# Performance work log

Hardware: AMD Instinct MI355X
Metric: run time of the kernel (lower is better)

The kernel has to match this reference:

```python
import jax, jax.numpy as jnp
import numpy as np

B, N, D, U = 8, 2048, 512, 128


def setup_inputs() -> dict:
    key = jax.random.key(0)
    k_x, k_q, k_k, k_v, k_o = jax.random.split(key, 5)
    scale_in = 1.0 / np.sqrt(D)
    scale_u = 1.0 / np.sqrt(U)
    return {
        "inputs": jax.random.normal(k_x, (B, N, D), dtype=jnp.float32),
        "W_q": jax.random.normal(k_q, (D, U), dtype=jnp.float32) * scale_in,
        "W_k": jax.random.normal(k_k, (D, U), dtype=jnp.float32) * scale_in,
        "W_v": jax.random.normal(k_v, (D, U), dtype=jnp.float32) * scale_in,
        "W_o": jax.random.normal(k_o, (U, D), dtype=jnp.float32) * scale_u,
        "b_o": jnp.zeros((D,), dtype=jnp.float32),
    }


def reference(inputs, W_q, W_k, W_v, W_o, b_o):
    # Single-head scaled dot-product self-attention + output dense + residual
    Q = jnp.einsum('bnd,du->bnu', inputs, W_q)
    K = jnp.einsum('bnd,du->bnu', inputs, W_k)
    V = jnp.einsum('bnd,du->bnu', inputs, W_v)
    inv_sqrt_u = 1.0 / jnp.sqrt(jnp.asarray(W_q.shape[-1], inputs.dtype))
    scores = jnp.einsum('bnu,bmu->bnm', Q, K) * inv_sqrt_u  # [B,N,N]
    attn = jax.nn.softmax(scores, axis=-1)
    ctx = jnp.einsum('bnm,bmu->bnu', attn, V)  # [B,N,U]
    return jnp.einsum('bnu,ud->bnd', ctx, W_o) + b_o + inputs
```

## Files before the change

kernel.cpp:

```cpp
#include <hip/hip_runtime.h>

#define BB 8
#define NN 2048
#define DD 512
#define UU 128
#define SPLITS 4
#define KSPLIT 512

typedef __bf16 bf16_t;
typedef __bf16 bf16x4 __attribute__((ext_vector_type(4)));
typedef __bf16 bf16x8 __attribute__((ext_vector_type(8)));
typedef float floatx4 __attribute__((ext_vector_type(4)));

__device__ __forceinline__ floatx4 mfma16(bf16x8 a, bf16x8 b, floatx4 c) {
  return __builtin_amdgcn_mfma_f32_16x16x32_bf16(a, b, c, 0, 0, 0);
}

#define SW(r, g) ((((g) ^ ((r) & 7)) * 8))

__device__ __forceinline__ void gld_lds16(const bf16_t* g, bf16_t* l) {
  __builtin_amdgcn_global_load_lds(
      (const __attribute__((address_space(1))) unsigned int*)g,
      (__attribute__((address_space(3))) unsigned int*)l, 16, 0, 0);
}

__global__ __launch_bounds__(256) void cast_x_kernel(const float* __restrict__ x,
                                                     bf16_t* __restrict__ xb) {
  int G = blockIdx.x * 256 + threadIdx.x;
  int token = G >> 6;
  int g = G & 63;
  int dstg = (g & 56) | ((g & 7) ^ (token & 7));
  const float4* src = reinterpret_cast<const float4*>(x) + (size_t)G * 2;
  float4 a = src[0], b = src[1];
  bf16x8 o;
  o[0] = (bf16_t)a.x; o[1] = (bf16_t)a.y; o[2] = (bf16_t)a.z; o[3] = (bf16_t)a.w;
  o[4] = (bf16_t)b.x; o[5] = (bf16_t)b.y; o[6] = (bf16_t)b.z; o[7] = (bf16_t)b.w;
  *reinterpret_cast<bf16x8*>(&xb[(size_t)token * 512 + dstg * 8]) = o;
}

__global__ __launch_bounds__(256) void pack_w_kernel(const float* __restrict__ wq,
                                                     const float* __restrict__ wk,
                                                     const float* __restrict__ wv,
                                                     const float* __restrict__ wo,
                                                     bf16_t* __restrict__ wqkvt,
                                                     bf16_t* __restrict__ wot) {
  int gid = blockIdx.x * 256 + threadIdx.x;
  if (gid < 384 * 512) {
    int nrow = gid >> 9;
    int kdst = gid & 511;
    int ksrc = (kdst & ~56) | (((((kdst >> 3) & 7)) ^ (nrow & 7)) << 3);
    const float* src = (nrow < 128) ? wq : ((nrow < 256) ? wk : wv);
    int n = nrow & 127;
    wqkvt[gid] = (bf16_t)src[ksrc * 128 + n];
  } else {
    int g = gid - 384 * 512;
    int nrow = g >> 7;
    int kdst = g & 127;
    int ksrc = (kdst & ~56) | (((((kdst >> 3) & 7)) ^ (nrow & 7)) << 3);
    wot[g] = (bf16_t)wo[ksrc * 512 + nrow];
  }
}

__global__ __launch_bounds__(256, 4) void qkv_gemm_kernel(const bf16_t* __restrict__ xb,
                                                          const bf16_t* __restrict__ wqkvt,
                                                          bf16_t* __restrict__ Q,
                                                          bf16_t* __restrict__ K,
                                                          bf16_t* __restrict__ Vt) {
  __shared__ bf16_t lA[128 * 64];
  __shared__ bf16_t lB[64 * 64];
  const int m0 = blockIdx.x * 128;
  const int n0 = blockIdx.y * 64;
  const int tid = threadIdx.x;
  const int w = tid >> 6, lane = tid & 63;
  const int quad = lane >> 4, l15 = lane & 15;

  floatx4 zero4 = {0.f, 0.f, 0.f, 0.f};
  floatx4 acc[2][4];
#pragma unroll
  for (int mi = 0; mi < 2; mi++)
#pragma unroll
    for (int nt = 0; nt < 4; nt++) acc[mi][nt] = zero4;

  for (int kc = 0; kc < 512; kc += 64) {
    __syncthreads();
#pragma unroll
    for (int i = 0; i < 4; i++) {
      int t = tid + i * 256;
      int r = t >> 3, g = t & 7;
      gld_lds16(&xb[(size_t)(m0 + r) * 512 + kc + g * 8], &lA[t * 8]);
    }
#pragma unroll
    for (int i = 0; i < 2; i++) {
      int t = tid + i * 256;
      int r = t >> 3, g = t & 7;
      gld_lds16(&wqkvt[(size_t)(n0 + r) * 512 + kc + g * 8], &lB[t * 8]);
    }
    asm volatile("s_waitcnt vmcnt(0)" ::: "memory");
    __syncthreads();
#pragma unroll
    for (int kb = 0; kb < 2; kb++) {
      bf16x8 bfr[4];
#pragma unroll
      for (int nt = 0; nt < 4; nt++)
        bfr[nt] = *reinterpret_cast<const bf16x8*>(
            &lB[(nt * 16 + l15) * 64 + SW(l15, kb * 4 + quad)]);
#pragma unroll
      for (int mi = 0; mi < 2; mi++) {
        bf16x8 a = *reinterpret_cast<const bf16x8*>(
            &lA[(w * 32 + mi * 16 + l15) * 64 + SW(l15, kb * 4 + quad)]);
#pragma unroll
        for (int nt = 0; nt < 4; nt++)
          acc[mi][nt] = mfma16(a, bfr[nt], acc[mi][nt]);
      }
    }
  }

#pragma unroll
  for (int mi = 0; mi < 2; mi++)
#pragma unroll
    for (int nt = 0; nt < 4; nt++) {
      int n = n0 + nt * 16 + l15;
#pragma unroll
      for (int r = 0; r < 4; r++) {
        int token = m0 + w * 32 + mi * 16 + quad * 4 + r;
        bf16_t h = (bf16_t)acc[mi][nt][r];
        if (n < 128) {
          Q[(size_t)token * 128 + n] = h;
        } else if (n < 256) {
          int nk = n - 128;
          int nsw = (nk & ~56) | ((((nk >> 3) & 7) ^ (token & 7)) << 3);
          K[(size_t)token * 128 + nsw] = h;
        } else {
          int bidx = token >> 11;
          int t = token & 2047;
          int u = n - 256;
          int tsw = (t & ~56) | ((((t >> 3) & 7) ^ (u & 7)) << 3);
          Vt[((size_t)bidx * 128 + u) * 2048 + tsw] = h;
        }
      }
    }
}

__global__ __launch_bounds__(256, 2) void attn_kernel(const bf16_t* __restrict__ Q,
                                                      const bf16_t* __restrict__ K,
                                                      const bf16_t* __restrict__ Vt,
                                                      bf16_t* __restrict__ Op,
                                                      float* __restrict__ ml) {
  __shared__ bf16_t lK[2][64 * 128];
  __shared__ bf16_t lV[2][128 * 64];
  __shared__ bf16_t lP[4][32 * 64];

  const int b = blockIdx.y;
  const int qb = blockIdx.x;
  const int s = blockIdx.z;
  const int tid = threadIdx.x;
  const int w = tid >> 6, lane = tid & 63;
  const int quad = lane >> 4, l15 = lane & 15;
  const float c = 0.08838834764831845f * 1.4426950408889634f;

  bf16x8 qf[2][4];
#pragma unroll
  for (int mt = 0; mt < 2; mt++) {
    const bf16_t* qrow =
        &Q[((size_t)b * NN + qb * 128 + w * 32 + mt * 16 + l15) * 128 + quad * 8];
#pragma unroll
    for (int kb = 0; kb < 4; kb++)
      qf[mt][kb] = *reinterpret_cast<const bf16x8*>(qrow + kb * 32);
  }

  float l_part[2] = {0.f, 0.f};
  floatx4 zero4 = {0.f, 0.f, 0.f, 0.f};
  floatx4 accO[2][8];
#pragma unroll
  for (int mt = 0; mt < 2; mt++)
#pragma unroll
    for (int ut = 0; ut < 8; ut++) accO[mt][ut] = zero4;

  bf16_t* pw = &lP[w][0];
  const int kt0 = s * KSPLIT;
  const bf16_t* kbase = &K[(size_t)b * NN * 128];
  const bf16_t* vbase = &Vt[(size_t)b * 128 * 2048];

  {
    const bf16_t* ksrc = kbase + (size_t)kt0 * 128;
#pragma unroll
    for (int i = 0; i < 4; i++) {
      int t = tid + i * 256;
      gld_lds16(ksrc + (size_t)t * 8, &lK[0][t * 8]);
    }
#pragma unroll
    for (int i = 0; i < 4; i++) {
      int t = tid + i * 256;
      int r = t >> 3, g = t & 7;
      gld_lds16(vbase + (size_t)r * 2048 + kt0 + g * 8, &lV[0][t * 8]);
    }
  }
  asm volatile("s_waitcnt vmcnt(0)" ::: "memory");
  __syncthreads();

  int cur = 0;
  for (int kt = kt0; kt < kt0 + KSPLIT; kt += 64) {
    if (kt + 64 < kt0 + KSPLIT) {
      const int nxt = kt + 64;
      const bf16_t* ksrc = kbase + (size_t)nxt * 128;
#pragma unroll
      for (int i = 0; i < 4; i++) {
        int t = tid + i * 256;
        gld_lds16(ksrc + (size_t)t * 8, &lK[cur ^ 1][t * 8]);
      }
#pragma unroll
      for (int i = 0; i < 4; i++) {
        int t = tid + i * 256;
        int r = t >> 3, g = t & 7;
        gld_lds16(vbase + (size_t)r * 2048 + nxt + g * 8, &lV[cur ^ 1][t * 8]);
      }
    }

    floatx4 accS[4][2];
#pragma unroll
    for (int km = 0; km < 4; km++)
#pragma unroll
      for (int mt = 0; mt < 2; mt++) accS[km][mt] = zero4;
    __builtin_amdgcn_s_setprio(1);
#pragma unroll
    for (int kb = 0; kb < 4; kb++) {
#pragma unroll
      for (int km = 0; km < 4; km++) {
        bf16x8 kf = *reinterpret_cast<const bf16x8*>(
            &lK[cur][(km * 16 + l15) * 128 + SW(l15, kb * 4 + quad)]);
#pragma unroll
        for (int mt = 0; mt < 2; mt++)
          accS[km][mt] = mfma16(kf, qf[mt][kb], accS[km][mt]);
      }
    }
    __builtin_amdgcn_s_setprio(0);

#pragma unroll
    for (int km = 0; km < 4; km++) {
#pragma unroll
      for (int mt = 0; mt < 2; mt++) {
        float p0 = __builtin_amdgcn_exp2f(accS[km][mt][0] * c);
        float p1 = __builtin_amdgcn_exp2f(accS[km][mt][1] * c);
        float p2 = __builtin_amdgcn_exp2f(accS[km][mt][2] * c);
        float p3 = __builtin_amdgcn_exp2f(accS[km][mt][3] * c);
        l_part[mt] += (p0 + p1) + (p2 + p3);
        bf16x4 pk;
        pk[0] = (bf16_t)p0; pk[1] = (bf16_t)p1; pk[2] = (bf16_t)p2; pk[3] = (bf16_t)p3;
        int row = mt * 16 + l15;
        int g = km * 2 + (quad >> 1);
        *reinterpret_cast<bf16x4*>(
            &pw[row * 64 + ((g ^ (row & 7)) * 8) + (quad & 1) * 4]) = pk;
      }
    }
    asm volatile("s_waitcnt lgkmcnt(0)" ::: "memory");

    __builtin_amdgcn_s_setprio(1);
#pragma unroll
    for (int kb = 0; kb < 2; kb++) {
      bf16x8 pa[2];
#pragma unroll
      for (int mt = 0; mt < 2; mt++)
        pa[mt] = *reinterpret_cast<const bf16x8*>(
            &pw[(mt * 16 + l15) * 64 + SW(l15, kb * 4 + quad)]);
#pragma unroll
      for (int ut = 0; ut < 8; ut++) {
        bf16x8 bv = *reinterpret_cast<const bf16x8*>(
            &lV[cur][(ut * 16 + l15) * 64 + SW(l15, kb * 4 + quad)]);
#pragma unroll
        for (int mt = 0; mt < 2; mt++)
          accO[mt][ut] = mfma16(pa[mt], bv, accO[mt][ut]);
      }
    }
    __builtin_amdgcn_s_setprio(0);

    asm volatile("s_waitcnt vmcnt(0)" ::: "memory");
    __syncthreads();
    cur ^= 1;
  }

#pragma unroll
  for (int mt = 0; mt < 2; mt++) {
    float v = l_part[mt];
    v += __shfl_xor(v, 16);
    v += __shfl_xor(v, 32);
    l_part[mt] = v;
  }

  size_t base = ((size_t)(b * 16 + qb) * SPLITS + s);
  bf16_t* op = Op + base * (128 * 128);
  float* mlp = ml + base * 128;
#pragma unroll
  for (int mt = 0; mt < 2; mt++)
#pragma unroll
    for (int ut = 0; ut < 8; ut++)
#pragma unroll
      for (int r = 0; r < 4; r++)
        op[(w * 32 + mt * 16 + quad * 4 + r) * 128 + ut * 16 + l15] =
            (bf16_t)accO[mt][ut][r];
  if (quad == 0) {
#pragma unroll
    for (int mt = 0; mt < 2; mt++) mlp[w * 32 + mt * 16 + l15] = l_part[mt];
  }
}

__global__ __launch_bounds__(256) void merge_kernel(const bf16_t* __restrict__ Op,
                                                    const float* __restrict__ ml,
                                                    bf16_t* __restrict__ ctx) {
  const int blk = blockIdx.x;
  const int q = threadIdx.x >> 1;
  const int u0 = blockIdx.y * 64 + (threadIdx.x & 1) * 32;

  float L = 0.f;
  float o[32];
#pragma unroll
  for (int j = 0; j < 32; j++) o[j] = 0.f;
#pragma unroll
  for (int s = 0; s < SPLITS; s++) {
    L += ml[((size_t)blk * SPLITS + s) * 128 + q];
    const bf16_t* op = Op + ((size_t)blk * SPLITS + s) * 16384 + q * 128 + u0;
#pragma unroll
    for (int v = 0; v < 4; v++) {
      bf16x8 ch = *reinterpret_cast<const bf16x8*>(op + v * 8);
#pragma unroll
      for (int j = 0; j < 8; j++) o[v * 8 + j] += (float)ch[j];
    }
  }
  float inv = 1.0f / L;
  const int bb = blk >> 4, qbl = blk & 15;
  bf16_t* dst = ctx + ((size_t)bb * NN + qbl * 128 + q) * 128;
#pragma unroll
  for (int v = 0; v < 4; v++) {
    int g = (u0 >> 3) + v;
    int gsw = (g & 8) | ((g & 7) ^ (q & 7));
    bf16x8 ch;
#pragma unroll
    for (int j = 0; j < 8; j++) ch[j] = (bf16_t)(o[v * 8 + j] * inv);
    *reinterpret_cast<bf16x8*>(dst + gsw * 8) = ch;
  }
}

__global__ __launch_bounds__(256, 4) void out_gemm_kernel(const bf16_t* __restrict__ ctx,
                                                          const bf16_t* __restrict__ wot,
                                                          const float* __restrict__ bo,
                                                          const float* __restrict__ x0,
                                                          float* __restrict__ out) {
  __shared__ bf16_t lA[64 * 128];
  __shared__ bf16_t lB[64 * 128];
  const int m0 = blockIdx.x * 64;
  const int n0 = blockIdx.y * 64;
  const int tid = threadIdx.x;
  const int w = tid >> 6, lane = tid & 63;
  const int quad = lane >> 4, l15 = lane & 15;

#pragma unroll
  for (int i = 0; i < 4; i++) {
    int t = tid + i * 256;
    gld_lds16(&ctx[(size_t)m0 * 128 + t * 8], &lA[t * 8]);
    gld_lds16(&wot[(size_t)n0 * 128 + t * 8], &lB[t * 8]);
  }
  asm volatile("s_waitcnt vmcnt(0)" ::: "memory");
  __syncthreads();

  floatx4 zero4 = {0.f, 0.f, 0.f, 0.f};
  floatx4 acc[4];
#pragma unroll
  for (int nt = 0; nt < 4; nt++) acc[nt] = zero4;
#pragma unroll
  for (int kb = 0; kb < 4; kb++) {
    bf16x8 a = *reinterpret_cast<const bf16x8*>(&lA[(w * 16 + l15) * 128 + SW(l15, kb * 4 + quad)]);
#pragma unroll
    for (int nt = 0; nt < 4; nt++) {
      bf16x8 bfr = *reinterpret_cast<const bf16x8*>(&lB[(nt * 16 + l15) * 128 + SW(l15, kb * 4 + quad)]);
      acc[nt] = mfma16(a, bfr, acc[nt]);
    }
  }

#pragma unroll
  for (int nt = 0; nt < 4; nt++) {
    int n = n0 + nt * 16 + l15;
    float bias = bo[n];
#pragma unroll
    for (int r = 0; r < 4; r++) {
      size_t m = m0 + w * 16 + quad * 4 + r;
      out[m * 512 + n] = acc[nt][r] + bias + x0[m * 512 + n];
    }
  }
}

extern "C" void kernel_launch(void* const* d_in, const int* in_sizes, int n_in,
                              void* d_out, int out_size, void* d_ws, size_t ws_size,
                              hipStream_t stream) {
  const float* x  = (const float*)d_in[0];
  const float* wq = (const float*)d_in[1];
  const float* wk = (const float*)d_in[2];
  const float* wv = (const float*)d_in[3];
  const float* wo = (const float*)d_in[4];
  const float* bo = (const float*)d_in[5];
  float* out = (float*)d_out;

  char* ws = (char*)d_ws;
  bf16_t* Qb    = (bf16_t*)(ws);
  bf16_t* Kb    = (bf16_t*)(ws + 4194304);
  bf16_t* Vt    = (bf16_t*)(ws + 2 * 4194304);
  bf16_t* Ctx   = (bf16_t*)(ws + 3 * 4194304);
  bf16_t* Wqkvt = (bf16_t*)(ws + 4 * 4194304);
  bf16_t* Wot   = (bf16_t*)(ws + 4 * 4194304 + 393216);
  bf16_t* Xb    = (bf16_t*)(ws + 4 * 4194304 + 524288);
  bf16_t* Op    = (bf16_t*)(ws + 4 * 4194304 + 524288);
  float*  ml    = (float*)(ws + 4 * 4194304 + 524288 + 33554432);

  cast_x_kernel<<<4096, 256, 0, stream>>>(x, Xb);
  pack_w_kernel<<<1024, 256, 0, stream>>>(wq, wk, wv, wo, Wqkvt, Wot);
  qkv_gemm_kernel<<<dim3(128, 6), 256, 0, stream>>>(Xb, Wqkvt, Qb, Kb, Vt);
  attn_kernel<<<dim3(16, 8, SPLITS), 256, 0, stream>>>(Qb, Kb, Vt, Op, ml);
  merge_kernel<<<dim3(128, 2), 256, 0, stream>>>(Op, ml, Ctx);
  out_gemm_kernel<<<dim3(256, 8), 256, 0, stream>>>(Ctx, Wot, bo, x, out);
}
```

Baseline: 147.6 us.

## Warp-specialize attention into QK/softmax producers and PV consumer waves

The attention kernel now runs 512 threads per block over 256 query rows. Four producer waves compute QK^T and exp for tile t+1 into a double-buffered P tile in LDS, while four consumer waves run P·V for tile t. K is staged two tiles ahead and V one tile ahead. The goal is to overlap softmax/exp work with the PV MFMAs and to halve K/V reloads per query, at the cost of more LDS, a 256-wide query block (half the grid) and a reworked merge kernel with finer per-thread work.

```diff
diff --git a/kernel.cpp b/kernel.cpp
--- a/kernel.cpp
+++ b/kernel.cpp
@@ -6,6 +6,7 @@
 #define UU 128
 #define SPLITS 4
 #define KSPLIT 512
+#define NT (KSPLIT / 64)
 
 typedef __bf16 bf16_t;
 typedef __bf16 bf16x4 __attribute__((ext_vector_type(4)));
@@ -141,14 +142,14 @@
     }
 }
 
-__global__ __launch_bounds__(256, 2) void attn_kernel(const bf16_t* __restrict__ Q,
+__global__ __launch_bounds__(512, 2) void attn_kernel(const bf16_t* __restrict__ Q,
                                                       const bf16_t* __restrict__ K,
                                                       const bf16_t* __restrict__ Vt,
                                                       bf16_t* __restrict__ Op,
                                                       float* __restrict__ ml) {
   __shared__ bf16_t lK[2][64 * 128];
   __shared__ bf16_t lV[2][128 * 64];
-  __shared__ bf16_t lP[4][32 * 64];
+  __shared__ bf16_t lP[2][256 * 64];
 
   const int b = blockIdx.y;
   const int qb = blockIdx.x;
@@ -156,150 +157,153 @@
   const int tid = threadIdx.x;
   const int w = tid >> 6, lane = tid & 63;
   const int quad = lane >> 4, l15 = lane & 15;
+  const int rw = w & 3;
+  const bool producer = (w < 4);
   const float c = 0.08838834764831845f * 1.4426950408889634f;
 
-  bf16x8 qf[2][4];
-#pragma unroll
-  for (int mt = 0; mt < 2; mt++) {
-    const bf16_t* qrow =
-        &Q[((size_t)b * NN + qb * 128 + w * 32 + mt * 16 + l15) * 128 + quad * 8];
-#pragma unroll
-    for (int kb = 0; kb < 4; kb++)
-      qf[mt][kb] = *reinterpret_cast<const bf16x8*>(qrow + kb * 32);
-  }
-
-  float l_part[2] = {0.f, 0.f};
+  const int kt0 = s * KSPLIT;
+  const bf16_t* kbase = &K[((size_t)b * NN + kt0) * 128];
+  const bf16_t* vbase = &Vt[(size_t)b * 128 * 2048 + kt0];
+
+  bf16x8 qf[4][4];
+  if (producer) {
+#pragma unroll
+    for (int mt = 0; mt < 4; mt++) {
+      const bf16_t* qrow =
+          &Q[((size_t)b * NN + qb * 256 + rw * 64 + mt * 16 + l15) * 128 + quad * 8];
+#pragma unroll
+      for (int kb = 0; kb < 4; kb++)
+        qf[mt][kb] = *reinterpret_cast<const bf16x8*>(qrow + kb * 32);
+    }
+  }
+
+  float l_part[4] = {0.f, 0.f, 0.f, 0.f};
   floatx4 zero4 = {0.f, 0.f, 0.f, 0.f};
-  floatx4 accO[2][8];
-#pragma unroll
-  for (int mt = 0; mt < 2; mt++)
+  floatx4 accO[4][8];
+#pragma unroll
+  for (int mt = 0; mt < 4; mt++)
 #pragma unroll
     for (int ut = 0; ut < 8; ut++) accO[mt][ut] = zero4;
 
-  bf16_t* pw = &lP[w][0];
-  const int kt0 = s * KSPLIT;
-  const bf16_t* kbase = &K[(size_t)b * NN * 128];
-  const bf16_t* vbase = &Vt[(size_t)b * 128 * 2048];
-
-  {
-    const bf16_t* ksrc = kbase + (size_t)kt0 * 128;
-#pragma unroll
-    for (int i = 0; i < 4; i++) {
-      int t = tid + i * 256;
-      gld_lds16(ksrc + (size_t)t * 8, &lK[0][t * 8]);
-    }
-#pragma unroll
-    for (int i = 0; i < 4; i++) {
-      int t = tid + i * 256;
-      int r = t >> 3, g = t & 7;
-      gld_lds16(vbase + (size_t)r * 2048 + kt0 + g * 8, &lV[0][t * 8]);
-    }
-  }
-  asm volatile("s_waitcnt vmcnt(0)" ::: "memory");
-  __syncthreads();
-
-  int cur = 0;
-  for (int kt = kt0; kt < kt0 + KSPLIT; kt += 64) {
-    if (kt + 64 < kt0 + KSPLIT) {
-      const int nxt = kt + 64;
-      const bf16_t* ksrc = kbase + (size_t)nxt * 128;
-#pragma unroll
-      for (int i = 0; i < 4; i++) {
-        int t = tid + i * 256;
-        gld_lds16(ksrc + (size_t)t * 8, &lK[cur ^ 1][t * 8]);
+  auto stageK = [&](int t) {
+    const bf16_t* src = kbase + (size_t)t * 64 * 128;
+    bf16_t* dst = lK[t & 1];
+#pragma unroll
+    for (int i = 0; i < 2; i++) {
+      int g = tid + i * 512;
+      gld_lds16(src + (size_t)g * 8, dst + g * 8);
+    }
+  };
+  auto stageV = [&](int t) {
+    bf16_t* dst = lV[t & 1];
+#pragma unroll
+    for (int i = 0; i < 2; i++) {
+      int g = tid + i * 512;
+      int r = g >> 3, gg = g & 7;
+      gld_lds16(vbase + (size_t)r * 2048 + t * 64 + gg * 8, dst + g * 8);
+    }
+  };
+
+  auto computeP = [&](int tt) {
+    const bf16_t* kl = lK[tt & 1];
+    bf16_t* pb = &lP[tt & 1][rw * 64 * 64];
+#pragma unroll
+    for (int km = 0; km < 4; km++) {
+      floatx4 accS[4];
+#pragma unroll
+      for (int mt = 0; mt < 4; mt++) accS[mt] = zero4;
+      __builtin_amdgcn_s_setprio(1);
+#pragma unroll
+      for (int kb = 0; kb < 4; kb++) {
+        bf16x8 kf = *reinterpret_cast<const bf16x8*>(
+            &kl[(km * 16 + l15) * 128 + SW(l15, kb * 4 + quad)]);
+#pragma unroll
+        for (int mt = 0; mt < 4; mt++)
+          accS[mt] = mfma16(kf, qf[mt][kb], accS[mt]);
       }
-#pragma unroll
-      for (int i = 0; i < 4; i++) {
-        int t = tid + i * 256;
-        int r = t >> 3, g = t & 7;
-        gld_lds16(vbase + (size_t)r * 2048 + nxt + g * 8, &lV[cur ^ 1][t * 8]);
-      }
-    }
-
-    floatx4 accS[4][2];
-#pragma unroll
-    for (int km = 0; km < 4; km++)
-#pragma unroll
-      for (int mt = 0; mt < 2; mt++) accS[km][mt] = zero4;
-    __builtin_amdgcn_s_setprio(1);
-#pragma unroll
-    for (int kb = 0; kb < 4; kb++) {
-#pragma unroll
-      for (int km = 0; km < 4; km++) {
-        bf16x8 kf = *reinterpret_cast<const bf16x8*>(
-            &lK[cur][(km * 16 + l15) * 128 + SW(l15, kb * 4 + quad)]);
-#pragma unroll
-        for (int mt = 0; mt < 2; mt++)
-          accS[km][mt] = mfma16(kf, qf[mt][kb], accS[km][mt]);
-      }
-    }
-    __builtin_amdgcn_s_setprio(0);
-
-#pragma unroll
-    for (int km = 0; km < 4; km++) {
-#pragma unroll
-      for (int mt = 0; mt < 2; mt++) {
-        float p0 = __builtin_amdgcn_exp2f(accS[km][mt][0] * c);
-        float p1 = __builtin_amdgcn_exp2f(accS[km][mt][1] * c);
-        float p2 = __builtin_amdgcn_exp2f(accS[km][mt][2] * c);
-        float p3 = __builtin_amdgcn_exp2f(accS[km][mt][3] * c);
+      __builtin_amdgcn_s_setprio(0);
+#pragma unroll
+      for (int mt = 0; mt < 4; mt++) {
+        float p0 = __builtin_amdgcn_exp2f(accS[mt][0] * c);
+        float p1 = __builtin_amdgcn_exp2f(accS[mt][1] * c);
+        float p2 = __builtin_amdgcn_exp2f(accS[mt][2] * c);
+        float p3 = __builtin_amdgcn_exp2f(accS[mt][3] * c);
         l_part[mt] += (p0 + p1) + (p2 + p3);
         bf16x4 pk;
         pk[0] = (bf16_t)p0; pk[1] = (bf16_t)p1; pk[2] = (bf16_t)p2; pk[3] = (bf16_t)p3;
         int row = mt * 16 + l15;
         int g = km * 2 + (quad >> 1);
         *reinterpret_cast<bf16x4*>(
-            &pw[row * 64 + ((g ^ (row & 7)) * 8) + (quad & 1) * 4]) = pk;
+            &pb[row * 64 + ((g ^ (row & 7)) * 8) + (quad & 1) * 4]) = pk;
       }
     }
-    asm volatile("s_waitcnt lgkmcnt(0)" ::: "memory");
-
-    __builtin_amdgcn_s_setprio(1);
-#pragma unroll
-    for (int kb = 0; kb < 2; kb++) {
-      bf16x8 pa[2];
-#pragma unroll
-      for (int mt = 0; mt < 2; mt++)
-        pa[mt] = *reinterpret_cast<const bf16x8*>(
-            &pw[(mt * 16 + l15) * 64 + SW(l15, kb * 4 + quad)]);
-#pragma unroll
-      for (int ut = 0; ut < 8; ut++) {
-        bf16x8 bv = *reinterpret_cast<const bf16x8*>(
-            &lV[cur][(ut * 16 + l15) * 64 + SW(l15, kb * 4 + quad)]);
-#pragma unroll
-        for (int mt = 0; mt < 2; mt++)
-          accO[mt][ut] = mfma16(pa[mt], bv, accO[mt][ut]);
+  };
+
+  stageK(0);
+  stageV(0);
+  stageK(1);
+  asm volatile("s_waitcnt vmcnt(0)" ::: "memory");
+  __syncthreads();
+  if (producer) computeP(0);
+  __syncthreads();
+
+  for (int t = 0; t < NT; ++t) {
+    if (t + 2 < NT) stageK(t + 2);
+    if (t + 1 < NT) stageV(t + 1);
+
+    if (producer) {
+      if (t + 1 < NT) computeP(t + 1);
+    } else {
+      const bf16_t* pbc = &lP[t & 1][rw * 64 * 64];
+      const bf16_t* vl = lV[t & 1];
+      __builtin_amdgcn_s_setprio(1);
+#pragma unroll
+      for (int kb = 0; kb < 2; kb++) {
+        bf16x8 pa[4];
+#pragma unroll
+        for (int mt = 0; mt < 4; mt++)
+          pa[mt] = *reinterpret_cast<const bf16x8*>(
+              &pbc[(mt * 16 + l15) * 64 + SW(l15, kb * 4 + quad)]);
+#pragma unroll
+        for (int ut = 0; ut < 8; ut++) {
+          bf16x8 bv = *reinterpret_cast<const bf16x8*>(
+              &vl[(ut * 16 + l15) * 64 + SW(l15, kb * 4 + quad)]);
+#pragma unroll
+          for (int mt = 0; mt < 4; mt++)
+            accO[mt][ut] = mfma16(pa[mt], bv, accO[mt][ut]);
+        }
       }
-    }
-    __builtin_amdgcn_s_setprio(0);
+      __builtin_amdgcn_s_setprio(0);
+    }
 
     asm volatile("s_waitcnt vmcnt(0)" ::: "memory");
     __syncthreads();
-    cur ^= 1;
-  }
-
-#pragma unroll
-  for (int mt = 0; mt < 2; mt++) {
-    float v = l_part[mt];
-    v += __shfl_xor(v, 16);
-    v += __shfl_xor(v, 32);
-    l_part[mt] = v;
-  }
-
-  size_t base = ((size_t)(b * 16 + qb) * SPLITS + s);
-  bf16_t* op = Op + base * (128 * 128);
-  float* mlp = ml + base * 128;
-#pragma unroll
-  for (int mt = 0; mt < 2; mt++)
-#pragma unroll
-    for (int ut = 0; ut < 8; ut++)
-#pragma unroll
-      for (int r = 0; r < 4; r++)
-        op[(w * 32 + mt * 16 + quad * 4 + r) * 128 + ut * 16 + l15] =
-            (bf16_t)accO[mt][ut][r];
-  if (quad == 0) {
-#pragma unroll
-    for (int mt = 0; mt < 2; mt++) mlp[w * 32 + mt * 16 + l15] = l_part[mt];
+  }
+
+  size_t base = ((size_t)(b * 8 + qb) * SPLITS + s);
+  if (producer) {
+#pragma unroll
+    for (int mt = 0; mt < 4; mt++) {
+      float v = l_part[mt];
+      v += __shfl_xor(v, 16);
+      v += __shfl_xor(v, 32);
+      l_part[mt] = v;
+    }
+    if (quad == 0) {
+      float* mlp = ml + base * 256 + rw * 64;
+#pragma unroll
+      for (int mt = 0; mt < 4; mt++) mlp[mt * 16 + l15] = l_part[mt];
+    }
+  } else {
+    bf16_t* op = Op + base * (256 * 128) + (size_t)rw * 64 * 128;
+#pragma unroll
+    for (int mt = 0; mt < 4; mt++)
+#pragma unroll
+      for (int ut = 0; ut < 8; ut++)
+#pragma unroll
+        for (int r = 0; r < 4; r++)
+          op[(mt * 16 + quad * 4 + r) * 128 + ut * 16 + l15] =
+              (bf16_t)accO[mt][ut][r];
   }
 }
 
@@ -307,36 +311,29 @@
                                                     const float* __restrict__ ml,
                                                     bf16_t* __restrict__ ctx) {
   const int blk = blockIdx.x;
-  const int q = threadIdx.x >> 1;
-  const int u0 = blockIdx.y * 64 + (threadIdx.x & 1) * 32;
+  const int qloc = blockIdx.y * 16 + (threadIdx.x >> 4);
+  const int g = threadIdx.x & 15;
 
   float L = 0.f;
-  float o[32];
-#pragma unroll
-  for (int j = 0; j < 32; j++) o[j] = 0.f;
+  float o[8];
+#pragma unroll
+  for (int j = 0; j < 8; j++) o[j] = 0.f;
 #pragma unroll
   for (int s = 0; s < SPLITS; s++) {
-    L += ml[((size_t)blk * SPLITS + s) * 128 + q];
-    const bf16_t* op = Op + ((size_t)blk * SPLITS + s) * 16384 + q * 128 + u0;
-#pragma unroll
-    for (int v = 0; v < 4; v++) {
-      bf16x8 ch = *reinterpret_cast<const bf16x8*>(op + v * 8);
-#pragma unroll
-      for (int j = 0; j < 8; j++) o[v * 8 + j] += (float)ch[j];
-    }
+    size_t e = (size_t)blk * SPLITS + s;
+    L += ml[e * 256 + qloc];
+    bf16x8 ch = *reinterpret_cast<const bf16x8*>(&Op[(e * 256 + qloc) * 128 + g * 8]);
+#pragma unroll
+    for (int j = 0; j < 8; j++) o[j] += (float)ch[j];
   }
   float inv = 1.0f / L;
-  const int bb = blk >> 4, qbl = blk & 15;
-  bf16_t* dst = ctx + ((size_t)bb * NN + qbl * 128 + q) * 128;
-#pragma unroll
-  for (int v = 0; v < 4; v++) {
-    int g = (u0 >> 3) + v;
-    int gsw = (g & 8) | ((g & 7) ^ (q & 7));
-    bf16x8 ch;
-#pragma unroll
-    for (int j = 0; j < 8; j++) ch[j] = (bf16_t)(o[v * 8 + j] * inv);
-    *reinterpret_cast<bf16x8*>(dst + gsw * 8) = ch;
-  }
+  int gsw = (g & 8) | ((g & 7) ^ (qloc & 7));
+  bf16x8 ch;
+#pragma unroll
+  for (int j = 0; j < 8; j++) ch[j] = (bf16_t)(o[j] * inv);
+  const int bb = blk >> 3, qbl = blk & 7;
+  *reinterpret_cast<bf16x8*>(
+      &ctx[((size_t)bb * NN + qbl * 256 + qloc) * 128 + gsw * 8]) = ch;
 }
 
 __global__ __launch_bounds__(256, 4) void out_gemm_kernel(const bf16_t* __restrict__ ctx,
@@ -412,7 +409,7 @@
   cast_x_kernel<<<4096, 256, 0, stream>>>(x, Xb);
   pack_w_kernel<<<1024, 256, 0, stream>>>(wq, wk, wv, wo, Wqkvt, Wot);
   qkv_gemm_kernel<<<dim3(128, 6), 256, 0, stream>>>(Xb, Wqkvt, Qb, Kb, Vt);
-  attn_kernel<<<dim3(16, 8, SPLITS), 256, 0, stream>>>(Qb, Kb, Vt, Op, ml);
-  merge_kernel<<<dim3(128, 2), 256, 0, stream>>>(Op, ml, Ctx);
+  attn_kernel<<<dim3(8, 8, SPLITS), 512, 0, stream>>>(Qb, Kb, Vt, Op, ml);
+  merge_kernel<<<dim3(64, 16), 256, 0, stream>>>(Op, ml, Ctx);
   out_gemm_kernel<<<dim3(256, 8), 256, 0, stream>>>(Ctx, Wot, bo, x, out);
 }
```

New measurement: 198.1 us. +34.2%, slower.
